# Optimization experiments

Hardware: AMD Instinct MI355X
Metric: run time of the kernel (lower is better)

The kernel has to match this reference:

```python
import jax, jax.numpy as jnp
import numpy as np


def setup_inputs() -> dict:
    key = jax.random.key(0)
    k1, k2, k3 = jax.random.split(key, 3)
    B, C_in, C_out, T = 16, 512, 512, 4096
    pre = jax.random.normal(k1, (B, C_in, T), dtype=jnp.float32)
    # nn.Linear weight layout: [out_features, in_features]
    W_pre = jax.random.normal(k2, (C_out, C_in), dtype=jnp.float32) * (1.0 / np.sqrt(C_in))
    b_pre = jax.random.normal(k3, (C_out,), dtype=jnp.float32) * 0.01
    return {"pre": pre, "W_pre": W_pre, "b_pre": b_pre}


def reference(pre, W_pre, b_pre):
    # Original 'casual' branch loops over T applying w_pre(_pre[:,:,i]) into BOTH
    # embedding_prev and embedding_curr, then sums -> 2 * (W_pre @ pre + b).
    # Batched form: one einsum over the full sequence.
    y = jnp.einsum('bct,oc->bot', pre, W_pre) + b_pre[None, :, None]  # [B, C_out, T]
    return y + y
```

## Files before the change

kernel.cpp:

```cpp
#include <hip/hip_runtime.h>
#include <hip/hip_bf16.h>

typedef __attribute__((ext_vector_type(8))) short short8_t;
typedef __attribute__((ext_vector_type(4))) float f32x4;

#define BATCH 16
#define CIN   512
#define COUT  512
#define TT    4096
#define BK    128
#define NKT   (CIN / BK)

__device__ __forceinline__ uint pk2(float a, float b) {
    ushort lo = __builtin_bit_cast(ushort, __float2bfloat16(a));
    ushort hi = __builtin_bit_cast(ushort, __float2bfloat16(b));
    return (uint)lo | ((uint)hi << 16);
}

extern "C" __global__ __launch_bounds__(256)
void wconv(const float* __restrict__ W, ushort* __restrict__ Wb)
{
    const int i  = blockIdx.x * 256 + threadIdx.x;
    const int m  = i >> 7;
    const int k0 = (i & 127) * 4;
    const float4 v = *(const float4*)(W + (size_t)m * CIN + k0);
    const int bm = m >> 4, r = m & 15;
    const int ksg = k0 >> 5, g = (k0 >> 3) & 3, k7 = k0 & 7;
    uint2 q;
    q.x = pk2(v.x, v.y);
    q.y = pk2(v.z, v.w);
    *(uint2*)&Wb[(size_t)bm * 8192 + ksg * 512 + g * 128 + r * 8 + k7] = q;
}

template<bool WSB>
__global__ __launch_bounds__(256)
void conv2x1_gemm(const float* __restrict__ pre, const float* __restrict__ W,
                  const ushort* __restrict__ Wb,
                  const float* __restrict__ bias, float* __restrict__ out)
{
    __shared__ alignas(16) ushort LB[2][16 * 512];

    const int tid  = threadIdx.x;
    const int lane = tid & 63;
    const int wm   = tid >> 6;
    const int g    = lane >> 4;
    const int l15  = lane & 15;

    const int id   = ((blockIdx.x & 7) << 9) | (blockIdx.x >> 3);
    const int mblk = id & 3;
    const int ti   = (id >> 2) & 63;
    const int bb   = id >> 8;

    const int m0 = mblk << 7;
    const int t0 = ti << 6;

    const float* preB   = pre + (size_t)bb * ((size_t)CIN * TT);
    const int    bmBase = (m0 >> 4) + wm * 2;

    const int b_p  = tid >> 4;
    const int b_tg = tid & 15;
    const int k0   = b_p << 3;

    float4   braw[8];
    short8_t af[4][2];

    f32x4 acc[2][4];
#pragma unroll
    for (int i = 0; i < 2; ++i)
#pragma unroll
        for (int j = 0; j < 4; ++j) acc[i][j] = (f32x4)0.0f;

#define LOAD_A(KT) do { \
    if constexpr (WSB) { \
        _Pragma("unroll") \
        for (int ks = 0; ks < 4; ++ks) \
            _Pragma("unroll") \
            for (int mi = 0; mi < 2; ++mi) \
                af[ks][mi] = *(const short8_t*)(Wb + (size_t)(bmBase + mi) * 8192 \
                                                + ((KT)*4 + ks) * 512 + g * 128 + l15 * 8); \
    } else { \
        _Pragma("unroll") \
        for (int ks = 0; ks < 4; ++ks) \
            _Pragma("unroll") \
            for (int mi = 0; mi < 2; ++mi) { \
                const float* ab = W + (size_t)(m0 + wm*32 + mi*16 + l15) * CIN \
                                  + (KT)*BK + ks*32 + g*8; \
                const float4 u0 = *(const float4*)ab; \
                const float4 u1 = *(const float4*)(ab + 4); \
                uint4 qq; \
                qq.x = pk2(u0.x, u0.y); qq.y = pk2(u0.z, u0.w); \
                qq.z = pk2(u1.x, u1.y); qq.w = pk2(u1.z, u1.w); \
                af[ks][mi] = __builtin_bit_cast(short8_t, qq); \
            } \
    } } while (0)

#define LOAD_B(KT) do { \
    _Pragma("unroll") \
    for (int j = 0; j < 8; ++j) \
        braw[j] = *(const float4*)(preB + (size_t)((KT)*BK + k0 + j) * TT + t0 + 4*b_tg); \
    } while (0)

#define CVT_WRITE(BUF) do { \
    _Pragma("unroll") \
    for (int jt = 0; jt < 4; ++jt) { \
        uint4 q; \
        q.x = pk2(((const float*)&braw[0])[jt], ((const float*)&braw[1])[jt]); \
        q.y = pk2(((const float*)&braw[2])[jt], ((const float*)&braw[3])[jt]); \
        q.z = pk2(((const float*)&braw[4])[jt], ((const float*)&braw[5])[jt]); \
        q.w = pk2(((const float*)&braw[6])[jt], ((const float*)&braw[7])[jt]); \
        const int n  = 4*b_tg + jt; \
        const int np = n ^ ((n >> 3) & 7); \
        *(uint4*)&LB[BUF][b_p * 512 + np * 8] = q; \
    } } while (0)

#define COMPUTE(BUF) do { \
    _Pragma("unroll") \
    for (int ks = 0; ks < 4; ++ks) { \
        short8_t bf[4]; \
        _Pragma("unroll") \
        for (int ni = 0; ni < 4; ++ni) { \
            const int n  = ni*16 + l15; \
            const int np = n ^ ((n >> 3) & 7); \
            bf[ni] = *(const short8_t*)&LB[BUF][(ks*4 + g) * 512 + np * 8]; \
        } \
        _Pragma("unroll") \
        for (int mi = 0; mi < 2; ++mi) \
            _Pragma("unroll") \
            for (int ni = 0; ni < 4; ++ni) \
                acc[mi][ni] = __builtin_amdgcn_mfma_f32_16x16x32_bf16(af[ks][mi], bf[ni], acc[mi][ni], 0, 0, 0); \
    } } while (0)

    LOAD_B(0);
    CVT_WRITE(0);
    __syncthreads();

#pragma unroll
    for (int kt = 0; kt < NKT; ++kt) {
        LOAD_A(kt);
        if (kt + 1 < NKT) LOAD_B(kt + 1);
        if (kt & 1) COMPUTE(1); else COMPUTE(0);
        if (kt + 1 < NKT) {
            if (kt & 1) CVT_WRITE(0); else CVT_WRITE(1);
            __syncthreads();
        }
    }

    const int orow = m0 + wm*32 + g*4;
    float bv[2][4];
#pragma unroll
    for (int mi = 0; mi < 2; ++mi)
#pragma unroll
        for (int r = 0; r < 4; ++r)
            bv[mi][r] = bias[orow + mi*16 + r];

    float* outB = out + (size_t)bb * ((size_t)COUT * TT);
#pragma unroll
    for (int mi = 0; mi < 2; ++mi) {
#pragma unroll
        for (int ni = 0; ni < 4; ++ni) {
            const int t = t0 + ni*16 + l15;
#pragma unroll
            for (int r = 0; r < 4; ++r) {
                const int o = orow + mi*16 + r;
                outB[(size_t)o * TT + t] = 2.0f * (acc[mi][ni][r] + bv[mi][r]);
            }
        }
    }
}

extern "C" void kernel_launch(void* const* d_in, const int* in_sizes, int n_in,
                              void* d_out, int out_size, void* d_ws, size_t ws_size,
                              hipStream_t stream)
{
    const float* pre  = (const float*)d_in[0];
    const float* Wp   = (const float*)d_in[1];
    const float* bias = (const float*)d_in[2];
    float* out = (float*)d_out;

    const bool usews = (ws_size >= (size_t)(COUT * CIN * sizeof(ushort)));

    if (usews) {
        ushort* Wb = (ushort*)d_ws;
        hipLaunchKernelGGL(wconv, dim3(256), dim3(256), 0, stream, Wp, Wb);
        hipLaunchKernelGGL((conv2x1_gemm<true>), dim3(BATCH * 4 * 64), dim3(256), 0, stream,
                           pre, Wp, Wb, bias, out);
    } else {
        hipLaunchKernelGGL((conv2x1_gemm<false>), dim3(BATCH * 4 * 64), dim3(256), 0, stream,
                           pre, Wp, (const ushort*)nullptr, bias, out);
    }
}
```

Baseline: 77.96 us.

## Halve K tile and prefetch B two stages ahead with register double-buffering

Reduces the K tile from 128 to 64 and keeps two register buffers of raw B data so global loads are issued two iterations ahead of their use. It also software-pipelines the weight fragment loads one step ahead, replaces __syncthreads with an explicit lgkmcnt wait plus s_barrier, and adds sched_barriers to fix instruction order. The LDS swizzle is simplified to match the new layout. The aim is deeper hiding of global memory latency, paid for with more barriers per K and a smaller per-thread load width (float2 instead of float4).

```diff
diff --git a/kernel.cpp b/kernel.cpp
--- a/kernel.cpp
+++ b/kernel.cpp
@@ -8,13 +8,20 @@
 #define CIN   512
 #define COUT  512
 #define TT    4096
-#define BK    128
+#define BK    64
 #define NKT   (CIN / BK)
 
 __device__ __forceinline__ uint pk2(float a, float b) {
     ushort lo = __builtin_bit_cast(ushort, __float2bfloat16(a));
     ushort hi = __builtin_bit_cast(ushort, __float2bfloat16(b));
     return (uint)lo | ((uint)hi << 16);
+}
+
+__device__ __forceinline__ void barrier_seq() {
+    asm volatile("s_waitcnt lgkmcnt(0)" ::: "memory");
+    __builtin_amdgcn_sched_barrier(0);
+    __builtin_amdgcn_s_barrier();
+    __builtin_amdgcn_sched_barrier(0);
 }
 
 extern "C" __global__ __launch_bounds__(256)
@@ -38,7 +45,7 @@
                   const ushort* __restrict__ Wb,
                   const float* __restrict__ bias, float* __restrict__ out)
 {
-    __shared__ alignas(16) ushort LB[2][16 * 512];
+    __shared__ alignas(16) ushort LB[2][8 * 64 * 8];
 
     const int tid  = threadIdx.x;
     const int lane = tid & 63;
@@ -57,12 +64,11 @@
     const float* preB   = pre + (size_t)bb * ((size_t)CIN * TT);
     const int    bmBase = (m0 >> 4) + wm * 2;
 
-    const int b_p  = tid >> 4;
-    const int b_tg = tid & 15;
-    const int k0   = b_p << 3;
-
-    float4   braw[8];
-    short8_t af[4][2];
+    const int b_p  = tid >> 5;
+    const int b_tq = tid & 31;
+
+    float2   brA[8], brB[8];
+    short8_t af[2][2];
 
     f32x4 acc[2][4];
 #pragma unroll
@@ -73,14 +79,14 @@
 #define LOAD_A(KT) do { \
     if constexpr (WSB) { \
         _Pragma("unroll") \
-        for (int ks = 0; ks < 4; ++ks) \
+        for (int ks = 0; ks < 2; ++ks) \
             _Pragma("unroll") \
             for (int mi = 0; mi < 2; ++mi) \
                 af[ks][mi] = *(const short8_t*)(Wb + (size_t)(bmBase + mi) * 8192 \
-                                                + ((KT)*4 + ks) * 512 + g * 128 + l15 * 8); \
+                                                + ((KT)*2 + ks) * 512 + g * 128 + l15 * 8); \
     } else { \
         _Pragma("unroll") \
-        for (int ks = 0; ks < 4; ++ks) \
+        for (int ks = 0; ks < 2; ++ks) \
             _Pragma("unroll") \
             for (int mi = 0; mi < 2; ++mi) { \
                 const float* ab = W + (size_t)(m0 + wm*32 + mi*16 + l15) * CIN \
@@ -94,34 +100,35 @@
             } \
     } } while (0)
 
-#define LOAD_B(KT) do { \
+#define LOAD_B(KT, BR) do { \
     _Pragma("unroll") \
     for (int j = 0; j < 8; ++j) \
-        braw[j] = *(const float4*)(preB + (size_t)((KT)*BK + k0 + j) * TT + t0 + 4*b_tg); \
+        BR[j] = *(const float2*)(preB + (size_t)((KT)*BK + b_p*8 + j) * TT + t0 + 2*b_tq); \
     } while (0)
 
-#define CVT_WRITE(BUF) do { \
+#define CVT_WRITE(BUF, BR) do { \
     _Pragma("unroll") \
-    for (int jt = 0; jt < 4; ++jt) { \
+    for (int tt = 0; tt < 2; ++tt) { \
         uint4 q; \
-        q.x = pk2(((const float*)&braw[0])[jt], ((const float*)&braw[1])[jt]); \
-        q.y = pk2(((const float*)&braw[2])[jt], ((const float*)&braw[3])[jt]); \
-        q.z = pk2(((const float*)&braw[4])[jt], ((const float*)&braw[5])[jt]); \
-        q.w = pk2(((const float*)&braw[6])[jt], ((const float*)&braw[7])[jt]); \
-        const int n  = 4*b_tg + jt; \
-        const int np = n ^ ((n >> 3) & 7); \
+        q.x = pk2(((const float*)&BR[0])[tt], ((const float*)&BR[1])[tt]); \
+        q.y = pk2(((const float*)&BR[2])[tt], ((const float*)&BR[3])[tt]); \
+        q.z = pk2(((const float*)&BR[4])[tt], ((const float*)&BR[5])[tt]); \
+        q.w = pk2(((const float*)&BR[6])[tt], ((const float*)&BR[7])[tt]); \
+        const int n  = 2*b_tq + tt; \
+        const int np = n ^ (b_p & 1); \
         *(uint4*)&LB[BUF][b_p * 512 + np * 8] = q; \
     } } while (0)
 
 #define COMPUTE(BUF) do { \
     _Pragma("unroll") \
-    for (int ks = 0; ks < 4; ++ks) { \
+    for (int ks = 0; ks < 2; ++ks) { \
         short8_t bf[4]; \
         _Pragma("unroll") \
         for (int ni = 0; ni < 4; ++ni) { \
             const int n  = ni*16 + l15; \
-            const int np = n ^ ((n >> 3) & 7); \
-            bf[ni] = *(const short8_t*)&LB[BUF][(ks*4 + g) * 512 + np * 8]; \
+            const int p  = ks*4 + g; \
+            const int np = n ^ (p & 1); \
+            bf[ni] = *(const short8_t*)&LB[BUF][p * 512 + np * 8]; \
         } \
         _Pragma("unroll") \
         for (int mi = 0; mi < 2; ++mi) \
@@ -130,18 +137,24 @@
                 acc[mi][ni] = __builtin_amdgcn_mfma_f32_16x16x32_bf16(af[ks][mi], bf[ni], acc[mi][ni], 0, 0, 0); \
     } } while (0)
 
-    LOAD_B(0);
-    CVT_WRITE(0);
-    __syncthreads();
+    LOAD_A(0);
+    LOAD_B(0, brA);
+    LOAD_B(1, brB);
+    CVT_WRITE(0, brA);
+    barrier_seq();
 
 #pragma unroll
     for (int kt = 0; kt < NKT; ++kt) {
-        LOAD_A(kt);
-        if (kt + 1 < NKT) LOAD_B(kt + 1);
-        if (kt & 1) COMPUTE(1); else COMPUTE(0);
+        if ((kt & 1) == 0) { if (kt + 2 < NKT) LOAD_B(kt + 2, brA); }
+        else               { if (kt + 2 < NKT) LOAD_B(kt + 2, brB); }
+        __builtin_amdgcn_sched_barrier(0);
+        if ((kt & 1) == 0) COMPUTE(0); else COMPUTE(1);
+        if (kt + 1 < NKT) LOAD_A(kt + 1);
+        __builtin_amdgcn_sched_barrier(0);
         if (kt + 1 < NKT) {
-            if (kt & 1) CVT_WRITE(0); else CVT_WRITE(1);
-            __syncthreads();
+            if ((kt & 1) == 0) CVT_WRITE(1, brB);
+            else               CVT_WRITE(0, brA);
+            barrier_seq();
         }
     }
 
```

Result: slower. 84.31 us (+8.1%).

## Stage fp32 activations via direct global-to-LDS loads with triple buffering

Applied to the files above, without the earlier changes.

Activation tiles now go straight from global memory into LDS as fp32 using global_load_lds, with no register staging. A three-deep ring of 64-wide K tiles keeps up to three stages in flight, and explicit vmcnt waits and barriers order them. The bf16 conversion moves from the producer into the compute loop, where each lane reads eight scalar fp32 values from a swizzled layout. Weight fragments are double-buffered in registers. The aim is to hide global load latency and free registers, at the cost of more LDS read instructions and conversion work in the MFMA loop, plus twice the LDS footprint.

```diff
diff --git a/kernel.cpp b/kernel.cpp
--- a/kernel.cpp
+++ b/kernel.cpp
@@ -8,14 +8,22 @@
 #define CIN   512
 #define COUT  512
 #define TT    4096
-#define BK    128
-#define NKT   (CIN / BK)
+#define BKT   64
+#define NKT   (CIN / BKT)
 
 __device__ __forceinline__ uint pk2(float a, float b) {
     ushort lo = __builtin_bit_cast(ushort, __float2bfloat16(a));
     ushort hi = __builtin_bit_cast(ushort, __float2bfloat16(b));
     return (uint)lo | ((uint)hi << 16);
 }
+
+#define SCHEDB() __builtin_amdgcn_sched_barrier(0)
+#define WAIT_VM4() do { asm volatile("s_waitcnt vmcnt(4)" ::: "memory"); SCHEDB(); } while (0)
+#define BARRIER() do { SCHEDB(); __builtin_amdgcn_s_barrier(); SCHEDB(); } while (0)
+
+#define GLOAD_LDS16(G, L) \
+    __builtin_amdgcn_global_load_lds((const __attribute__((address_space(1))) void*)(G), \
+                                     (__attribute__((address_space(3))) void*)(L), 16, 0, 0)
 
 extern "C" __global__ __launch_bounds__(256)
 void wconv(const float* __restrict__ W, ushort* __restrict__ Wb)
@@ -38,11 +46,11 @@
                   const ushort* __restrict__ Wb,
                   const float* __restrict__ bias, float* __restrict__ out)
 {
-    __shared__ alignas(16) ushort LB[2][16 * 512];
+    __shared__ float LBUF[3 * 4096];
 
     const int tid  = threadIdx.x;
     const int lane = tid & 63;
-    const int wm   = tid >> 6;
+    const int wv   = tid >> 6;
     const int g    = lane >> 4;
     const int l15  = lane & 15;
 
@@ -55,14 +63,9 @@
     const int t0 = ti << 6;
 
     const float* preB   = pre + (size_t)bb * ((size_t)CIN * TT);
-    const int    bmBase = (m0 >> 4) + wm * 2;
+    const int    bmBase = (m0 >> 4) + wv * 2;
 
-    const int b_p  = tid >> 4;
-    const int b_tg = tid & 15;
-    const int k0   = b_p << 3;
-
-    float4   braw[8];
-    short8_t af[4][2];
+    short8_t afA[2][2], afB[2][2];
 
     f32x4 acc[2][4];
 #pragma unroll
@@ -70,82 +73,84 @@
 #pragma unroll
         for (int j = 0; j < 4; ++j) acc[i][j] = (f32x4)0.0f;
 
-#define LOAD_A(KT) do { \
+#define STAGE(KT, BUF) do { \
+    _Pragma("unroll") \
+    for (int i = 0; i < 4; ++i) { \
+        const int kb = wv*16 + i*4; \
+        const int k  = kb + (lane >> 4); \
+        const int sw = (((((KT)*BKT + k) >> 3) * 5) & 7); \
+        const float* gsrc = preB + (size_t)((KT)*BKT + k) * TT + t0 \
+                            + (((lane & 15) ^ sw) << 2); \
+        float* ldst = &LBUF[(BUF)*4096 + kb*64 + (lane << 2)]; \
+        GLOAD_LDS16(gsrc, ldst); \
+    } } while (0)
+
+#define LOAD_A(KT, AF) do { \
     if constexpr (WSB) { \
         _Pragma("unroll") \
-        for (int ks = 0; ks < 4; ++ks) \
+        for (int ks = 0; ks < 2; ++ks) \
             _Pragma("unroll") \
             for (int mi = 0; mi < 2; ++mi) \
-                af[ks][mi] = *(const short8_t*)(Wb + (size_t)(bmBase + mi) * 8192 \
-                                                + ((KT)*4 + ks) * 512 + g * 128 + l15 * 8); \
+                AF[ks][mi] = *(const short8_t*)(Wb + (size_t)(bmBase + mi) * 8192 \
+                                                + ((KT)*2 + ks) * 512 + g * 128 + l15 * 8); \
     } else { \
         _Pragma("unroll") \
-        for (int ks = 0; ks < 4; ++ks) \
+        for (int ks = 0; ks < 2; ++ks) \
             _Pragma("unroll") \
             for (int mi = 0; mi < 2; ++mi) { \
-                const float* ab = W + (size_t)(m0 + wm*32 + mi*16 + l15) * CIN \
-                                  + (KT)*BK + ks*32 + g*8; \
+                const float* ab = W + (size_t)(m0 + wv*32 + mi*16 + l15) * CIN \
+                                  + (KT)*BKT + ks*32 + g*8; \
                 const float4 u0 = *(const float4*)ab; \
                 const float4 u1 = *(const float4*)(ab + 4); \
                 uint4 qq; \
                 qq.x = pk2(u0.x, u0.y); qq.y = pk2(u0.z, u0.w); \
                 qq.z = pk2(u1.x, u1.y); qq.w = pk2(u1.z, u1.w); \
-                af[ks][mi] = __builtin_bit_cast(short8_t, qq); \
+                AF[ks][mi] = __builtin_bit_cast(short8_t, qq); \
             } \
     } } while (0)
 
-#define LOAD_B(KT) do { \
+#define COMPUTE(BUF, AF) do { \
+    const float* bb0 = &LBUF[(BUF)*4096]; \
     _Pragma("unroll") \
-    for (int j = 0; j < 8; ++j) \
-        braw[j] = *(const float4*)(preB + (size_t)((KT)*BK + k0 + j) * TT + t0 + 4*b_tg); \
-    } while (0)
-
-#define CVT_WRITE(BUF) do { \
-    _Pragma("unroll") \
-    for (int jt = 0; jt < 4; ++jt) { \
-        uint4 q; \
-        q.x = pk2(((const float*)&braw[0])[jt], ((const float*)&braw[1])[jt]); \
-        q.y = pk2(((const float*)&braw[2])[jt], ((const float*)&braw[3])[jt]); \
-        q.z = pk2(((const float*)&braw[4])[jt], ((const float*)&braw[5])[jt]); \
-        q.w = pk2(((const float*)&braw[6])[jt], ((const float*)&braw[7])[jt]); \
-        const int n  = 4*b_tg + jt; \
-        const int np = n ^ ((n >> 3) & 7); \
-        *(uint4*)&LB[BUF][b_p * 512 + np * 8] = q; \
+    for (int ks = 0; ks < 2; ++ks) { \
+        _Pragma("unroll") \
+        for (int ni = 0; ni < 4; ++ni) { \
+            const int n4 = ni*4 + (l15 >> 2); \
+            const int sw = (((ks*4 + g) * 5) & 7); \
+            const float* bp = bb0 + (ks*32 + g*8)*64 + ((n4 ^ sw) << 2) + (l15 & 3); \
+            uint4 q; \
+            q.x = pk2(bp[0],   bp[64]); \
+            q.y = pk2(bp[128], bp[192]); \
+            q.z = pk2(bp[256], bp[320]); \
+            q.w = pk2(bp[384], bp[448]); \
+            const short8_t bf = __builtin_bit_cast(short8_t, q); \
+            _Pragma("unroll") \
+            for (int mi = 0; mi < 2; ++mi) \
+                acc[mi][ni] = __builtin_amdgcn_mfma_f32_16x16x32_bf16(AF[ks][mi], bf, acc[mi][ni], 0, 0, 0); \
+        } \
     } } while (0)
 
-#define COMPUTE(BUF) do { \
-    _Pragma("unroll") \
-    for (int ks = 0; ks < 4; ++ks) { \
-        short8_t bf[4]; \
-        _Pragma("unroll") \
-        for (int ni = 0; ni < 4; ++ni) { \
-            const int n  = ni*16 + l15; \
-            const int np = n ^ ((n >> 3) & 7); \
-            bf[ni] = *(const short8_t*)&LB[BUF][(ks*4 + g) * 512 + np * 8]; \
-        } \
-        _Pragma("unroll") \
-        for (int mi = 0; mi < 2; ++mi) \
-            _Pragma("unroll") \
-            for (int ni = 0; ni < 4; ++ni) \
-                acc[mi][ni] = __builtin_amdgcn_mfma_f32_16x16x32_bf16(af[ks][mi], bf[ni], acc[mi][ni], 0, 0, 0); \
-    } } while (0)
-
-    LOAD_B(0);
-    CVT_WRITE(0);
-    __syncthreads();
+    STAGE(0, 0);
+    LOAD_A(0, afA);
+    STAGE(1, 1);
+    STAGE(2, 2);
 
 #pragma unroll
     for (int kt = 0; kt < NKT; ++kt) {
-        LOAD_A(kt);
-        if (kt + 1 < NKT) LOAD_B(kt + 1);
-        if (kt & 1) COMPUTE(1); else COMPUTE(0);
+        const int cur = kt % 3;
+        WAIT_VM4();
+        BARRIER();
         if (kt + 1 < NKT) {
-            if (kt & 1) CVT_WRITE(0); else CVT_WRITE(1);
-            __syncthreads();
+            if ((kt & 1) == 0) LOAD_A(kt + 1, afB);
+            else               LOAD_A(kt + 1, afA);
         }
+        if ((kt & 1) == 0) COMPUTE(cur, afA);
+        else               COMPUTE(cur, afB);
+        BARRIER();
+        if (kt + 3 < NKT) STAGE(kt + 3, cur);
     }
 
-    const int orow = m0 + wm*32 + g*4;
+    const int orow = m0 + wv*32 + g*4;
     float bv[2][4];
 #pragma unroll
     for (int mi = 0; mi < 2; ++mi)
```

Measured after the change: 91.53 us. 17.4% more time.

## Load whole K-slice of activations into LDS once, retile to 256x32 blocks

Applied to the files above, without the earlier changes.

Replaces the double-buffered K-loop with a single upfront load of the full K=512 by 32-column activation slab into shared memory, converted to bf16, followed by one barrier and a sync-free MFMA loop over K. The block tile changes from 128x64 to 256x32 (two M blocks per T tile), so each block reads its activation columns once for the full output channel range. This removes the per-stage barriers and halves the redundant activation reads across M blocks. In exchange the load phase no longer overlaps with compute, weight fragments are fetched from global memory in every K step, and the narrower 32-wide T tile gives 64-byte row segments on loads and stores.

```diff
diff --git a/kernel.cpp b/kernel.cpp
--- a/kernel.cpp
+++ b/kernel.cpp
@@ -8,8 +8,6 @@
 #define CIN   512
 #define COUT  512
 #define TT    4096
-#define BK    128
-#define NKT   (CIN / BK)
 
 __device__ __forceinline__ uint pk2(float a, float b) {
     ushort lo = __builtin_bit_cast(ushort, __float2bfloat16(a));
@@ -38,130 +36,104 @@
                   const ushort* __restrict__ Wb,
                   const float* __restrict__ bias, float* __restrict__ out)
 {
-    __shared__ alignas(16) ushort LB[2][16 * 512];
+    __shared__ alignas(16) ushort LB[64 * 32 * 8];
 
     const int tid  = threadIdx.x;
     const int lane = tid & 63;
-    const int wm   = tid >> 6;
+    const int wv   = tid >> 6;
     const int g    = lane >> 4;
     const int l15  = lane & 15;
 
     const int id   = ((blockIdx.x & 7) << 9) | (blockIdx.x >> 3);
-    const int mblk = id & 3;
-    const int ti   = (id >> 2) & 63;
+    const int mblk = id & 1;
+    const int ti   = (id >> 1) & 127;
     const int bb   = id >> 8;
 
-    const int m0 = mblk << 7;
-    const int t0 = ti << 6;
+    const int m0 = mblk << 8;
+    const int t0 = ti << 5;
 
     const float* preB   = pre + (size_t)bb * ((size_t)CIN * TT);
-    const int    bmBase = (m0 >> 4) + wm * 2;
+    const int    bmBase = (m0 >> 4) + wv * 4;
 
-    const int b_p  = tid >> 4;
-    const int b_tg = tid & 15;
-    const int k0   = b_p << 3;
-
-    float4   braw[8];
-    short8_t af[4][2];
-
-    f32x4 acc[2][4];
 #pragma unroll
-    for (int i = 0; i < 2; ++i)
+    for (int it = 0; it < 2; ++it) {
+        const int slot = it * 256 + tid;
+        const int ko   = slot >> 3;
+        const int tg   = slot & 7;
+        float4 v[8];
 #pragma unroll
-        for (int j = 0; j < 4; ++j) acc[i][j] = (f32x4)0.0f;
-
-#define LOAD_A(KT) do { \
-    if constexpr (WSB) { \
-        _Pragma("unroll") \
-        for (int ks = 0; ks < 4; ++ks) \
-            _Pragma("unroll") \
-            for (int mi = 0; mi < 2; ++mi) \
-                af[ks][mi] = *(const short8_t*)(Wb + (size_t)(bmBase + mi) * 8192 \
-                                                + ((KT)*4 + ks) * 512 + g * 128 + l15 * 8); \
-    } else { \
-        _Pragma("unroll") \
-        for (int ks = 0; ks < 4; ++ks) \
-            _Pragma("unroll") \
-            for (int mi = 0; mi < 2; ++mi) { \
-                const float* ab = W + (size_t)(m0 + wm*32 + mi*16 + l15) * CIN \
-                                  + (KT)*BK + ks*32 + g*8; \
-                const float4 u0 = *(const float4*)ab; \
-                const float4 u1 = *(const float4*)(ab + 4); \
-                uint4 qq; \
-                qq.x = pk2(u0.x, u0.y); qq.y = pk2(u0.z, u0.w); \
-                qq.z = pk2(u1.x, u1.y); qq.w = pk2(u1.z, u1.w); \
-                af[ks][mi] = __builtin_bit_cast(short8_t, qq); \
-            } \
-    } } while (0)
-
-#define LOAD_B(KT) do { \
-    _Pragma("unroll") \
-    for (int j = 0; j < 8; ++j) \
-        braw[j] = *(const float4*)(preB + (size_t)((KT)*BK + k0 + j) * TT + t0 + 4*b_tg); \
-    } while (0)
-
-#define CVT_WRITE(BUF) do { \
-    _Pragma("unroll") \
-    for (int jt = 0; jt < 4; ++jt) { \
-        uint4 q; \
-        q.x = pk2(((const float*)&braw[0])[jt], ((const float*)&braw[1])[jt]); \
-        q.y = pk2(((const float*)&braw[2])[jt], ((const float*)&braw[3])[jt]); \
-        q.z = pk2(((const float*)&braw[4])[jt], ((const float*)&braw[5])[jt]); \
-        q.w = pk2(((const float*)&braw[6])[jt], ((const float*)&braw[7])[jt]); \
-        const int n  = 4*b_tg + jt; \
-        const int np = n ^ ((n >> 3) & 7); \
-        *(uint4*)&LB[BUF][b_p * 512 + np * 8] = q; \
-    } } while (0)
-
-#define COMPUTE(BUF) do { \
-    _Pragma("unroll") \
-    for (int ks = 0; ks < 4; ++ks) { \
-        short8_t bf[4]; \
-        _Pragma("unroll") \
-        for (int ni = 0; ni < 4; ++ni) { \
-            const int n  = ni*16 + l15; \
-            const int np = n ^ ((n >> 3) & 7); \
-            bf[ni] = *(const short8_t*)&LB[BUF][(ks*4 + g) * 512 + np * 8]; \
-        } \
-        _Pragma("unroll") \
-        for (int mi = 0; mi < 2; ++mi) \
-            _Pragma("unroll") \
-            for (int ni = 0; ni < 4; ++ni) \
-                acc[mi][ni] = __builtin_amdgcn_mfma_f32_16x16x32_bf16(af[ks][mi], bf[ni], acc[mi][ni], 0, 0, 0); \
-    } } while (0)
-
-    LOAD_B(0);
-    CVT_WRITE(0);
+        for (int j = 0; j < 8; ++j)
+            v[j] = *(const float4*)(preB + (size_t)(ko * 8 + j) * TT + t0 + tg * 4);
+#pragma unroll
+        for (int jj = 0; jj < 4; ++jj) {
+            uint4 q;
+            q.x = pk2(((const float*)&v[0])[jj], ((const float*)&v[1])[jj]);
+            q.y = pk2(((const float*)&v[2])[jj], ((const float*)&v[3])[jj]);
+            q.z = pk2(((const float*)&v[4])[jj], ((const float*)&v[5])[jj]);
+            q.w = pk2(((const float*)&v[6])[jj], ((const float*)&v[7])[jj]);
+            const int sl = (tg * 4 + jj) ^ (ko & 7);
+            *(uint4*)&LB[ko * 256 + sl * 8] = q;
+        }
+    }
     __syncthreads();
 
+    f32x4 acc[4][2];
 #pragma unroll
-    for (int kt = 0; kt < NKT; ++kt) {
-        LOAD_A(kt);
-        if (kt + 1 < NKT) LOAD_B(kt + 1);
-        if (kt & 1) COMPUTE(1); else COMPUTE(0);
-        if (kt + 1 < NKT) {
-            if (kt & 1) CVT_WRITE(0); else CVT_WRITE(1);
-            __syncthreads();
+    for (int i = 0; i < 4; ++i)
+#pragma unroll
+        for (int j = 0; j < 2; ++j) acc[i][j] = (f32x4)0.0f;
+
+#pragma unroll 4
+    for (int it = 0; it < 16; ++it) {
+        short8_t af[4], bf[2];
+        if constexpr (WSB) {
+#pragma unroll
+            for (int mi = 0; mi < 4; ++mi)
+                af[mi] = *(const short8_t*)(Wb + (size_t)(bmBase + mi) * 8192
+                                            + it * 512 + g * 128 + l15 * 8);
+        } else {
+#pragma unroll
+            for (int mi = 0; mi < 4; ++mi) {
+                const float* ab = W + (size_t)(m0 + wv * 64 + mi * 16 + l15) * CIN
+                                  + it * 32 + g * 8;
+                const float4 u0 = *(const float4*)ab;
+                const float4 u1 = *(const float4*)(ab + 4);
+                uint4 qq;
+                qq.x = pk2(u0.x, u0.y); qq.y = pk2(u0.z, u0.w);
+                qq.z = pk2(u1.x, u1.y); qq.w = pk2(u1.z, u1.w);
+                af[mi] = __builtin_bit_cast(short8_t, qq);
+            }
         }
+#pragma unroll
+        for (int ni = 0; ni < 2; ++ni) {
+            const int ko = it * 4 + g;
+            const int sl = (ni * 16 + l15) ^ (ko & 7);
+            bf[ni] = *(const short8_t*)&LB[ko * 256 + sl * 8];
+        }
+#pragma unroll
+        for (int mi = 0; mi < 4; ++mi)
+#pragma unroll
+            for (int ni = 0; ni < 2; ++ni)
+                acc[mi][ni] = __builtin_amdgcn_mfma_f32_16x16x32_bf16(af[mi], bf[ni], acc[mi][ni], 0, 0, 0);
     }
 
-    const int orow = m0 + wm*32 + g*4;
-    float bv[2][4];
+    const int orow = m0 + wv * 64 + g * 4;
+    float bv[4][4];
 #pragma unroll
-    for (int mi = 0; mi < 2; ++mi)
+    for (int mi = 0; mi < 4; ++mi)
 #pragma unroll
         for (int r = 0; r < 4; ++r)
-            bv[mi][r] = bias[orow + mi*16 + r];
+            bv[mi][r] = bias[orow + mi * 16 + r];
 
     float* outB = out + (size_t)bb * ((size_t)COUT * TT);
 #pragma unroll
-    for (int mi = 0; mi < 2; ++mi) {
+    for (int mi = 0; mi < 4; ++mi) {
 #pragma unroll
-        for (int ni = 0; ni < 4; ++ni) {
-            const int t = t0 + ni*16 + l15;
+        for (int ni = 0; ni < 2; ++ni) {
+            const int t = t0 + ni * 16 + l15;
 #pragma unroll
             for (int r = 0; r < 4; ++r) {
-                const int o = orow + mi*16 + r;
+                const int o = orow + mi * 16 + r;
                 outB[(size_t)o * TT + t] = 2.0f * (acc[mi][ni][r] + bv[mi][r]);
             }
         }
@@ -179,13 +151,16 @@
 
     const bool usews = (ws_size >= (size_t)(COUT * CIN * sizeof(ushort)));
 
+    const dim3 grid(BATCH * 2 * 128);
+    const dim3 block(256);
+
     if (usews) {
         ushort* Wb = (ushort*)d_ws;
         hipLaunchKernelGGL(wconv, dim3(256), dim3(256), 0, stream, Wp, Wb);
-        hipLaunchKernelGGL((conv2x1_gemm<true>), dim3(BATCH * 4 * 64), dim3(256), 0, stream,
+        hipLaunchKernelGGL((conv2x1_gemm<true>), grid, block, 0, stream,
                            pre, Wp, Wb, bias, out);
     } else {
-        hipLaunchKernelGGL((conv2x1_gemm<false>), dim3(BATCH * 4 * 64), dim3(256), 0, stream,
+        hipLaunchKernelGGL((conv2x1_gemm<false>), grid, block, 0, stream,
                            pre, Wp, (const ushort*)nullptr, bias, out);
     }
 }
```

Measured after the change: 93.04 us. +19.3%, slower.
